# Optimization experiments

Hardware: AMD Instinct MI355X
Metric: run time of the kernel (lower is better)

The kernel has to match this reference:

```python
import jax, jax.numpy as jnp
import numpy as np

SAMPLES = 16        # samples per spatial dim -> M = SAMPLES**2 sample points
SAMPLE_PAD = 0
K = 9               # nearest neighbors == conv kernel size == stride


def setup_inputs() -> dict:
    key = jax.random.key(0)
    k1, k2, k3 = jax.random.split(key, 3)
    B, C, H, W = 16, 128, 64, 64
    OUT = 128
    x = jax.random.normal(k1, (B, C, H, W), dtype=jnp.float32)
    w = jax.random.normal(k2, (OUT, C, K), dtype=jnp.float32) * 0.05
    b = jax.random.normal(k3, (OUT,), dtype=jnp.float32) * 0.05
    return {"x": x, "w": w, "b": b}


def reference(x, w, b):
    B, C, H, W = x.shape
    N = H * W
    # --- spatial sample grid (static, shape-derived) ---
    xi = jnp.round(jnp.linspace(SAMPLE_PAD, H - SAMPLE_PAD - 1, SAMPLES)).astype(jnp.int32)
    yi = jnp.round(jnp.linspace(SAMPLE_PAD, W - SAMPLE_PAD - 1, SAMPLES)).astype(jnp.int32)
    xg, yg = jnp.meshgrid(xi, yi, indexing='ij')
    x_sample = x[:, :, xg, yg].reshape(B, C, -1)          # (B, C, M)
    x1 = x.reshape(B, C, N)                                # (B, C, N)
    # --- squared Euclidean distance between tokens and samples ---
    dots = jnp.einsum('bcn,bcm->bnm', x1, x_sample)        # (B, N, M)
    n2 = jnp.sum(x1 * x1, axis=1)                          # (B, N)
    m2 = jnp.sum(x_sample * x_sample, axis=1)              # (B, M)
    dist2 = n2[:, :, None] + m2[:, None, :] - 2.0 * dots   # (B, N, M)
    # K nearest samples per token (smallest distance)
    _, idx = jax.lax.top_k(-dist2, K)                      # (B, N, K) int32
    # gather neighbor features from the sample set: (B, C, N, K)
    nbrs = jnp.take_along_axis(x_sample[:, :, None, :],
                               idx[:, None, :, :], axis=3)
    # Conv1d(kernel=K, stride=K) over the (B, C, N*K) prime tensor
    out = jnp.einsum('bcnk,ock->bon', nbrs, w) + b[None, :, None]
    return out.reshape(B, w.shape[0], H, W)
```

## Files before the change

kernel.cpp:

```cpp
#include <hip/hip_runtime.h>

#define NB   16
#define NC   128
#define NN   4096
#define NM   256
#define NK   9
#define NO   128

typedef __attribute__((ext_vector_type(8))) short bf16x8;
typedef __attribute__((ext_vector_type(4))) float f32x4;

__device__ __constant__ int d_grid16[16] = {0,4,8,13,17,21,25,29,34,38,42,46,50,55,59,63};

__device__ inline unsigned short bf16_rne(float v) {
    unsigned u = __float_as_uint(v);
    return (unsigned short)((u + 0x7FFFu + ((u >> 16) & 1u)) >> 16);
}

__device__ inline void merge16(unsigned* s, const unsigned* q) {
    unsigned r[16];
    #pragma unroll
    for (int i = 0; i < 16; ++i) r[i] = min(s[i], q[15 - i]);
    #pragma unroll
    for (int d = 8; d >= 1; d >>= 1)
        #pragma unroll
        for (int i = 0; i < 16; ++i)
            if (!(i & d)) { unsigned a = r[i], b2 = r[i + d]; r[i] = min(a, b2); r[i + d] = max(a, b2); }
    #pragma unroll
    for (int i = 0; i < 16; ++i) s[i] = r[i];
}

__global__ __launch_bounds__(256) void k_prep(const float* __restrict__ x,
                                              const float* __restrict__ w,
                                              float* __restrict__ xsT,
                                              unsigned short* __restrict__ xsTh,
                                              unsigned short* __restrict__ xsTl,
                                              unsigned short* __restrict__ Wth,
                                              unsigned short* __restrict__ Wtl,
                                              float* __restrict__ n2g,
                                              float* __restrict__ m2) {
    __shared__ float tile[16 * 260];
    int bx = blockIdx.x, t = threadIdx.x;
    if (bx < 128) {
        int b = bx >> 3, c0 = (bx & 7) * 16;
        int m = t;
        int pix = d_grid16[m >> 4] * 64 + d_grid16[m & 15];
        #pragma unroll
        for (int cc = 0; cc < 16; ++cc)
            tile[cc * 260 + m] = x[((size_t)b * NC + c0 + cc) * NN + pix];
        __syncthreads();
        #pragma unroll
        for (int e = 0; e < 4; ++e) {
            float fv[4];
            fv[0] = tile[(4 * e + 0) * 260 + m];
            fv[1] = tile[(4 * e + 1) * 260 + m];
            fv[2] = tile[(4 * e + 2) * 260 + m];
            fv[3] = tile[(4 * e + 3) * 260 + m];
            size_t base = ((size_t)b * NM + m) * NC + c0 + 4 * e;
            *(float4*)&xsT[base] = make_float4(fv[0], fv[1], fv[2], fv[3]);
            unsigned short h4[4], l4[4];
            #pragma unroll
            for (int e2 = 0; e2 < 4; ++e2) {
                unsigned short h = bf16_rne(fv[e2]);
                h4[e2] = h;
                l4[e2] = bf16_rne(fv[e2] - __uint_as_float(((unsigned)h) << 16));
            }
            *(ushort4*)&xsTh[base] = make_ushort4(h4[0], h4[1], h4[2], h4[3]);
            *(ushort4*)&xsTl[base] = make_ushort4(l4[0], l4[1], l4[2], l4[3]);
        }
    } else if (bx < 704) {
        int f = (bx - 128) * 256 + t;
        int ko = f >> 7, c = f & 127;
        int o = ko & 127, k = ko >> 7;
        float v = w[(size_t)o * 1152 + c * 9 + k];
        unsigned short h = bf16_rne(v);
        Wth[f] = h;
        Wtl[f] = bf16_rne(v - __uint_as_float(((unsigned)h) << 16));
    } else if (bx < 960) {
        #pragma clang fp contract(off)
        int i = bx - 704;
        int b = i >> 4, n = (i & 15) * 256 + t;
        const float* p = x + (size_t)b * NC * NN + n;
        float a = 0.f;
        #pragma unroll 16
        for (int c = 0; c < NC; ++c) { float v = p[(size_t)c * NN]; a = __fadd_rn(a, __fmul_rn(v, v)); }
        n2g[(size_t)b * NN + n] = a;
    } else {
        #pragma clang fp contract(off)
        int b = bx - 960;
        int pix = d_grid16[t >> 4] * 64 + d_grid16[t & 15];
        const float* p = x + (size_t)b * NC * NN + pix;
        float a = 0.f;
        #pragma unroll 16
        for (int c = 0; c < NC; ++c) { float v = p[(size_t)c * NN]; a = __fadd_rn(a, __fmul_rn(v, v)); }
        m2[b * NM + t] = a;
    }
}

__global__ __launch_bounds__(256) void k_g(const unsigned short* __restrict__ xsTh,
                                           const unsigned short* __restrict__ xsTl,
                                           const unsigned short* __restrict__ Wth,
                                           const unsigned short* __restrict__ Wtl,
                                           float* __restrict__ G) {
    int id = blockIdx.x;
    int b = id & 15, r = id >> 4;
    int kk = r % 9, mt = r / 9;
    int t = threadIdx.x;
    int w = t >> 6, lane = t & 63;
    int lr = lane & 15, quad = lane >> 4;
    int m = b * NM + mt * 64 + w * 16 + lr;
    const unsigned short* aph = xsTh + (size_t)m * NC;
    const unsigned short* apl = xsTl + (size_t)m * NC;
    f32x4 acc[8];
    #pragma unroll
    for (int j = 0; j < 8; ++j) acc[j] = (f32x4){0.f, 0.f, 0.f, 0.f};
    #pragma unroll
    for (int kb = 0; kb < 4; ++kb) {
        int co = kb * 32 + quad * 8;
        bf16x8 Ah = *(const bf16x8*)&aph[co];
        bf16x8 Al = *(const bf16x8*)&apl[co];
        #pragma unroll
        for (int j = 0; j < 8; ++j) {
            size_t wrow = ((size_t)kk * 128 + 16 * j + lr) * NC + co;
            bf16x8 Bh = *(const bf16x8*)&Wth[wrow];
            bf16x8 Bl = *(const bf16x8*)&Wtl[wrow];
            acc[j] = __builtin_amdgcn_mfma_f32_16x16x32_bf16(Ah, Bh, acc[j], 0, 0, 0);
            acc[j] = __builtin_amdgcn_mfma_f32_16x16x32_bf16(Al, Bh, acc[j], 0, 0, 0);
            acc[j] = __builtin_amdgcn_mfma_f32_16x16x32_bf16(Ah, Bl, acc[j], 0, 0, 0);
        }
    }
    int mrow = b * NM + mt * 64 + w * 16 + quad * 4;
    #pragma unroll
    for (int j = 0; j < 8; ++j)
        #pragma unroll
        for (int r2 = 0; r2 < 4; ++r2)
            G[((size_t)(mrow + r2)) * 1152 + kk * 128 + 16 * j + lr] = acc[j][r2];
}

__global__ __launch_bounds__(256, 2) void k_selref(const float* __restrict__ x,
                                                   const unsigned short* __restrict__ xsTh,
                                                   const unsigned short* __restrict__ xsTl,
                                                   const float* __restrict__ xsT,
                                                   const float* __restrict__ m2,
                                                   const float* __restrict__ n2g,
                                                   int* __restrict__ idx) {
    #pragma clang fp contract(off)
    __shared__ __align__(16) float x1l[32 * 132];
    __shared__ __align__(16) unsigned short xhp[32 * 136];
    __shared__ __align__(16) unsigned short xlp[32 * 136];
    __shared__ __align__(16) unsigned mrg[32 * 17 * 2];
    __shared__ unsigned short candl[32 * 16];
    __shared__ float m2l[256];
    __shared__ float n2l[32];
    unsigned* wl = mrg;
    unsigned long long* pairs = (unsigned long long*)mrg;

    int b = blockIdx.x & 15, n0 = (blockIdx.x >> 4) * 32;
    int t = threadIdx.x;
    int w = t >> 6, lane = t & 63;
    int lr = lane & 15, quad = lane >> 4;

    m2l[t] = m2[b * NM + t];
    if (t < 32) n2l[t] = n2g[(size_t)b * NN + n0 + t];

    #pragma unroll
    for (int it = 0; it < 4; ++it) {
        int f4 = it * 256 + t;
        int c = f4 >> 3, nn4 = (f4 & 7) * 4;
        float4 v = *(const float4*)&x[((size_t)b * NC + c) * NN + n0 + nn4];
        x1l[(nn4 + 0) * 132 + c] = v.x;
        x1l[(nn4 + 1) * 132 + c] = v.y;
        x1l[(nn4 + 2) * 132 + c] = v.z;
        x1l[(nn4 + 3) * 132 + c] = v.w;
    }
    __syncthreads();

    {
        int tok = t >> 3, c0 = (t & 7) * 16;
        #pragma unroll
        for (int g = 0; g < 4; ++g) {
            float4 v = *(const float4*)&x1l[tok * 132 + c0 + 4 * g];
            float vf[4] = {v.x, v.y, v.z, v.w};
            unsigned short h4[4], l4[4];
            #pragma unroll
            for (int e = 0; e < 4; ++e) {
                unsigned short h = bf16_rne(vf[e]);
                h4[e] = h;
                l4[e] = bf16_rne(vf[e] - __uint_as_float(((unsigned)h) << 16));
            }
            *(ushort4*)&xhp[tok * 136 + c0 + 4 * g] = make_ushort4(h4[0], h4[1], h4[2], h4[3]);
            *(ushort4*)&xlp[tok * 136 + c0 + 4 * g] = make_ushort4(l4[0], l4[1], l4[2], l4[3]);
        }
    }
    __syncthreads();

    f32x4 acc[2][4];
    #pragma unroll
    for (int i = 0; i < 2; ++i)
        #pragma unroll
        for (int j = 0; j < 4; ++j) acc[i][j] = (f32x4){0.f, 0.f, 0.f, 0.f};
    int mbase = w * 64;
    #pragma unroll
    for (int kb = 0; kb < 4; ++kb) {
        int co = kb * 32 + quad * 8;
        bf16x8 Bh0 = *(const bf16x8*)&xhp[lr * 136 + co];
        bf16x8 Bl0 = *(const bf16x8*)&xlp[lr * 136 + co];
        bf16x8 Bh1 = *(const bf16x8*)&xhp[(16 + lr) * 136 + co];
        bf16x8 Bl1 = *(const bf16x8*)&xlp[(16 + lr) * 136 + co];
        bf16x8 Ah[4], Al[4];
        #pragma unroll
        for (int j = 0; j < 4; ++j) {
            size_t arow = ((size_t)(b * NM + mbase + 16 * j + lr)) * NC + co;
            Ah[j] = *(const bf16x8*)&xsTh[arow];
            Al[j] = *(const bf16x8*)&xsTl[arow];
        }
        #pragma unroll
        for (int j = 0; j < 4; ++j) {
            acc[0][j] = __builtin_amdgcn_mfma_f32_16x16x32_bf16(Ah[j], Bh0, acc[0][j], 0, 0, 0);
            acc[0][j] = __builtin_amdgcn_mfma_f32_16x16x32_bf16(Ah[j], Bl0, acc[0][j], 0, 0, 0);
            acc[0][j] = __builtin_amdgcn_mfma_f32_16x16x32_bf16(Al[j], Bh0, acc[0][j], 0, 0, 0);
            acc[1][j] = __builtin_amdgcn_mfma_f32_16x16x32_bf16(Ah[j], Bh1, acc[1][j], 0, 0, 0);
            acc[1][j] = __builtin_amdgcn_mfma_f32_16x16x32_bf16(Ah[j], Bl1, acc[1][j], 0, 0, 0);
            acc[1][j] = __builtin_amdgcn_mfma_f32_16x16x32_bf16(Al[j], Bh1, acc[1][j], 0, 0, 0);
        }
    }

    #pragma unroll
    for (int h = 0; h < 2; ++h) {
        unsigned s16v[16];
        #pragma unroll
        for (int j = 0; j < 4; ++j)
            #pragma unroll
            for (int r = 0; r < 4; ++r) {
                int m = mbase + 16 * j + quad * 4 + r;
                float key = fmaf(-2.f, acc[h][j][r], m2l[m]);
                unsigned u = __float_as_uint(key);
                u = (u & 0x80000000u) ? ~u : (u | 0x80000000u);
                s16v[4 * j + r] = (u & 0xFFFFFF00u) | (unsigned)m;
            }
        #define CE(i,jx) { unsigned a_ = s16v[i], b_ = s16v[jx]; s16v[i] = min(a_, b_); s16v[jx] = max(a_, b_); }
        CE(0,1) CE(2,3) CE(0,2) CE(1,3) CE(1,2)
        CE(4,5) CE(6,7) CE(4,6) CE(5,7) CE(5,6)
        CE(0,4) CE(2,6) CE(2,4) CE(1,5) CE(3,7) CE(3,5) CE(1,2) CE(3,4) CE(5,6)
        CE(8,9) CE(10,11) CE(8,10) CE(9,11) CE(9,10)
        CE(12,13) CE(14,15) CE(12,14) CE(13,15) CE(13,14)
        CE(8,12) CE(10,14) CE(10,12) CE(9,13) CE(11,15) CE(11,13) CE(9,10) CE(11,12) CE(13,14)
        CE(0,8) CE(4,12) CE(4,8) CE(2,10) CE(6,14) CE(6,10) CE(2,4) CE(6,8) CE(10,12)
        CE(1,9) CE(5,13) CE(5,9) CE(3,11) CE(7,15) CE(7,11) CE(3,5) CE(7,9) CE(11,13)
        CE(1,2) CE(3,4) CE(5,6) CE(7,8) CE(9,10) CE(11,12) CE(13,14)
        #undef CE

        #pragma unroll
        for (int d = 16; d <= 32; d <<= 1) {
            unsigned q[16];
            #pragma unroll
            for (int i = 0; i < 16; ++i) q[i] = (unsigned)__shfl_xor((int)s16v[i], d, 64);
            merge16(s16v, q);
        }

        if (quad == 0) {
            #pragma unroll
            for (int ii = 0; ii < 4; ++ii)
                *(uint4*)&wl[(w * 16 + lr) * 16 + 4 * ii] =
                    make_uint4(s16v[4*ii], s16v[4*ii+1], s16v[4*ii+2], s16v[4*ii+3]);
        }
        __syncthreads();
        #pragma unroll
        for (int p = 1; p < 4; ++p) {
            int pw = (w + p) & 3;
            unsigned q[16];
            #pragma unroll
            for (int i = 0; i < 16; ++i) q[i] = wl[(pw * 16 + lr) * 16 + i];
            merge16(s16v, q);
        }
        if (w == 0 && quad == 0) {
            unsigned* c32 = (unsigned*)candl;
            #pragma unroll
            for (int i = 0; i < 16; i += 2)
                c32[(16 * h + lr) * 8 + (i >> 1)] =
                    (s16v[i] & 255u) | ((s16v[i + 1] & 255u) << 16);
        }
        __syncthreads();
    }

    {
        int tok = t >> 3, q8 = t & 7;
        float n2 = n2l[tok];
        int mym[2];
        unsigned long long myp[2];
        #pragma unroll
        for (int s = 0; s < 2; ++s) {
            int m = candl[tok * 16 + q8 + 8 * s];
            mym[s] = m;
            const float* xt = xsT + ((size_t)(b * NM + m)) * NC;
            float dot = 0.f;
            for (int c4 = 0; c4 < 32; ++c4) {
                float4 xv = *(const float4*)&x1l[tok * 132 + 4 * c4];
                float4 sv = *(const float4*)&xt[4 * c4];
                dot = __fadd_rn(dot, __fmul_rn(xv.x, sv.x));
                dot = __fadd_rn(dot, __fmul_rn(xv.y, sv.y));
                dot = __fadd_rn(dot, __fmul_rn(xv.z, sv.z));
                dot = __fadd_rn(dot, __fmul_rn(xv.w, sv.w));
            }
            float key = __fsub_rn(__fadd_rn(n2, m2l[m]), __fmul_rn(2.f, dot));
            unsigned u = __float_as_uint(key);
            u = (u & 0x80000000u) ? ~u : (u | 0x80000000u);
            myp[s] = ((unsigned long long)u << 32) | (unsigned)m;
            pairs[tok * 17 + q8 + 8 * s] = myp[s];
        }
        __syncthreads();
        unsigned long long pl[16];
        #pragma unroll
        for (int l2 = 0; l2 < 16; ++l2) pl[l2] = pairs[tok * 17 + l2];
        size_t obase = (size_t)(b * NN + n0 + tok) * NK;
        #pragma unroll
        for (int s = 0; s < 2; ++s) {
            int rank = 0;
            #pragma unroll
            for (int l2 = 0; l2 < 16; ++l2) rank += (pl[l2] < myp[s]);
            if (rank < 9) idx[obase + rank] = mym[s];
        }
    }
}

__global__ __launch_bounds__(256) void k_out(const float* __restrict__ G,
                                             const int* __restrict__ idx,
                                             const float* __restrict__ bias,
                                             float* __restrict__ out) {
    __shared__ float S[64 * 129];
    __shared__ int   idxl[576];
    __shared__ float biasl[128];
    int b = blockIdx.x & 15, n0 = (blockIdx.x >> 4) * 64;
    int t = threadIdx.x;
    if (t < 128) biasl[t] = bias[t];
    for (int f = t; f < 576; f += 256) idxl[f] = idx[(size_t)(b * NN + n0) * NK + f];
    __syncthreads();
    int o = t & 127, half = t >> 7;
    for (int p = 0; p < 32; ++p) {
        int n = p * 2 + half;
        float a = biasl[o];
        #pragma unroll
        for (int k = 0; k < 9; ++k) {
            int m = idxl[n * 9 + k];
            a += G[(((size_t)(b * NM + m)) * NK + k) * 128 + o];
        }
        S[n * 129 + o] = a;
    }
    __syncthreads();
    int nn = t & 63, ob = t >> 6;
    for (int p = 0; p < 32; ++p) {
        int o2 = p * 4 + ob;
        out[((size_t)(b * NO + o2)) * NN + n0 + nn] = S[nn * 129 + o2];
    }
}

extern "C" void kernel_launch(void* const* d_in, const int* in_sizes, int n_in,
                              void* d_out, int out_size, void* d_ws, size_t ws_size,
                              hipStream_t stream) {
    const float* x    = (const float*)d_in[0];
    const float* w    = (const float*)d_in[1];
    const float* bias = (const float*)d_in[2];
    float* out = (float*)d_out;

    float* ws   = (float*)d_ws;
    float* m2   = ws;
    float* n2g  = ws + 4096;
    float* xsT  = ws + 69632;
    float* G    = ws + 593920;
    int*   idx  = (int*)(ws + 5312512);
    unsigned short* xsTh = (unsigned short*)(ws + 5902336);
    unsigned short* xsTl = (unsigned short*)(ws + 6164480);
    unsigned short* Wth  = (unsigned short*)(ws + 6426624);
    unsigned short* Wtl  = (unsigned short*)(ws + 6500352);

    k_prep  <<<dim3(976),  dim3(256), 0, stream>>>(x, w, xsT, xsTh, xsTl, Wth, Wtl, n2g, m2);
    k_g     <<<dim3(576),  dim3(256), 0, stream>>>(xsTh, xsTl, Wth, Wtl, G);
    k_selref<<<dim3(2048), dim3(256), 0, stream>>>(x, xsTh, xsTl, xsT, m2, n2g, idx);
    k_out   <<<dim3(1024), dim3(256), 0, stream>>>(G, idx, bias, out);
}
```

Measured before the change: 232.4 us.

## Alias fp32 token tile with bf16 split buffers to cut shared memory

The fp32 token tile and the bf16 hi/lo split buffers now share one LDS region. The split is computed straight from the global loads, which removes one shared-memory pass and one barrier. The fp32 tile is reloaded from global memory after candidate selection for the exact rescoring step. The cross-wave merge now runs only in wave 0 rather than redundantly in all waves. The aim is to lower LDS footprint and redundant work so more blocks fit per CU, at the cost of a second global read of x and uncoalesced 2-byte transposed LDS stores.

```diff
diff --git a/kernel.cpp b/kernel.cpp
--- a/kernel.cpp
+++ b/kernel.cpp
@@ -145,13 +145,14 @@
                                                    const float* __restrict__ n2g,
                                                    int* __restrict__ idx) {
     #pragma clang fp contract(off)
-    __shared__ __align__(16) float x1l[32 * 132];
-    __shared__ __align__(16) unsigned short xhp[32 * 136];
-    __shared__ __align__(16) unsigned short xlp[32 * 136];
-    __shared__ __align__(16) unsigned mrg[32 * 17 * 2];
+    __shared__ __align__(16) unsigned char ubuf[17408];
+    __shared__ __align__(16) unsigned mrg[1088];
     __shared__ unsigned short candl[32 * 16];
     __shared__ float m2l[256];
     __shared__ float n2l[32];
+    unsigned short* xhp = (unsigned short*)ubuf;
+    unsigned short* xlp = xhp + 32 * 136;
+    float* xr = (float*)ubuf;
     unsigned* wl = mrg;
     unsigned long long* pairs = (unsigned long long*)mrg;
 
@@ -168,28 +169,13 @@
         int f4 = it * 256 + t;
         int c = f4 >> 3, nn4 = (f4 & 7) * 4;
         float4 v = *(const float4*)&x[((size_t)b * NC + c) * NN + n0 + nn4];
-        x1l[(nn4 + 0) * 132 + c] = v.x;
-        x1l[(nn4 + 1) * 132 + c] = v.y;
-        x1l[(nn4 + 2) * 132 + c] = v.z;
-        x1l[(nn4 + 3) * 132 + c] = v.w;
-    }
-    __syncthreads();
-
-    {
-        int tok = t >> 3, c0 = (t & 7) * 16;
-        #pragma unroll
-        for (int g = 0; g < 4; ++g) {
-            float4 v = *(const float4*)&x1l[tok * 132 + c0 + 4 * g];
-            float vf[4] = {v.x, v.y, v.z, v.w};
-            unsigned short h4[4], l4[4];
-            #pragma unroll
-            for (int e = 0; e < 4; ++e) {
-                unsigned short h = bf16_rne(vf[e]);
-                h4[e] = h;
-                l4[e] = bf16_rne(vf[e] - __uint_as_float(((unsigned)h) << 16));
-            }
-            *(ushort4*)&xhp[tok * 136 + c0 + 4 * g] = make_ushort4(h4[0], h4[1], h4[2], h4[3]);
-            *(ushort4*)&xlp[tok * 136 + c0 + 4 * g] = make_ushort4(l4[0], l4[1], l4[2], l4[3]);
+        float vf[4] = {v.x, v.y, v.z, v.w};
+        #pragma unroll
+        for (int e = 0; e < 4; ++e) {
+            unsigned short h = bf16_rne(vf[e]);
+            unsigned short l = bf16_rne(vf[e] - __uint_as_float(((unsigned)h) << 16));
+            xhp[(nn4 + e) * 136 + c] = h;
+            xlp[(nn4 + e) * 136 + c] = l;
         }
     }
     __syncthreads();
@@ -265,23 +251,36 @@
                     make_uint4(s16v[4*ii], s16v[4*ii+1], s16v[4*ii+2], s16v[4*ii+3]);
         }
         __syncthreads();
-        #pragma unroll
-        for (int p = 1; p < 4; ++p) {
-            int pw = (w + p) & 3;
-            unsigned q[16];
-            #pragma unroll
-            for (int i = 0; i < 16; ++i) q[i] = wl[(pw * 16 + lr) * 16 + i];
-            merge16(s16v, q);
-        }
-        if (w == 0 && quad == 0) {
-            unsigned* c32 = (unsigned*)candl;
-            #pragma unroll
-            for (int i = 0; i < 16; i += 2)
-                c32[(16 * h + lr) * 8 + (i >> 1)] =
-                    (s16v[i] & 255u) | ((s16v[i + 1] & 255u) << 16);
+        if (w == 0) {
+            #pragma unroll
+            for (int p = 1; p < 4; ++p) {
+                unsigned q[16];
+                #pragma unroll
+                for (int i = 0; i < 16; ++i) q[i] = wl[(p * 16 + lr) * 16 + i];
+                merge16(s16v, q);
+            }
+            if (quad == 0) {
+                unsigned* c32 = (unsigned*)candl;
+                #pragma unroll
+                for (int i = 0; i < 16; i += 2)
+                    c32[(16 * h + lr) * 8 + (i >> 1)] =
+                        (s16v[i] & 255u) | ((s16v[i + 1] & 255u) << 16);
+            }
         }
         __syncthreads();
     }
+
+    #pragma unroll
+    for (int it = 0; it < 4; ++it) {
+        int f4 = it * 256 + t;
+        int c = f4 >> 3, nn4 = (f4 & 7) * 4;
+        float4 v = *(const float4*)&x[((size_t)b * NC + c) * NN + n0 + nn4];
+        xr[(nn4 + 0) * 132 + c] = v.x;
+        xr[(nn4 + 1) * 132 + c] = v.y;
+        xr[(nn4 + 2) * 132 + c] = v.z;
+        xr[(nn4 + 3) * 132 + c] = v.w;
+    }
+    __syncthreads();
 
     {
         int tok = t >> 3, q8 = t & 7;
@@ -295,7 +294,7 @@
             const float* xt = xsT + ((size_t)(b * NM + m)) * NC;
             float dot = 0.f;
             for (int c4 = 0; c4 < 32; ++c4) {
-                float4 xv = *(const float4*)&x1l[tok * 132 + 4 * c4];
+                float4 xv = *(const float4*)&xr[tok * 132 + 4 * c4];
                 float4 sv = *(const float4*)&xt[4 * c4];
                 dot = __fadd_rn(dot, __fmul_rn(xv.x, sv.x));
                 dot = __fadd_rn(dot, __fmul_rn(xv.y, sv.y));
```

Measured after the change: 231.2 us. Within noise of the previous version (-0.5%).
